# Optimization experiments

Measured on AMD Instinct MI355X. Metric: run time of the kernel, lower is better.

Reference implementation:

```python
import jax, jax.numpy as jnp
import numpy as np

COMMITMENT_COST = 0.25
NUM_EMBEDDINGS = 1024
EMBEDDING_DIM = 256


def setup_inputs() -> dict:
    key = jax.random.key(0)
    k1, k2 = jax.random.split(key)
    inputs = jax.random.normal(k1, (64, 256, 32, 32), dtype=jnp.float32)
    emb_w = jax.random.normal(k2, (NUM_EMBEDDINGS, EMBEDDING_DIM), dtype=jnp.float32)
    return {"inputs": inputs, "emb_w": emb_w}


def reference(inputs, emb_w):
    # NCHW -> NHWC, flatten to [N, D]
    x = jnp.transpose(inputs, (0, 2, 3, 1))  # [B, H, W, D]
    B, H, W, D = x.shape
    flat = x.reshape(-1, D)  # [N, D]

    distances = (
        jnp.sum(flat * flat, axis=1, keepdims=True)
        + jnp.sum(emb_w * emb_w, axis=1)
        - 2.0 * flat @ emb_w.T
    )
    idx = jnp.argmin(distances, axis=1)  # [N]

    # one-hot @ W is just a gather of codebook rows
    quantized = emb_w[idx].reshape(B, H, W, D)

    # avg_probs = mean of one-hot encodings = normalized codeword counts
    counts = jnp.zeros((NUM_EMBEDDINGS,), dtype=jnp.float32).at[idx].add(1.0)
    avg_probs = counts / flat.shape[0]
    perplexity = jnp.exp(-jnp.sum(avg_probs * jnp.log(avg_probs + 1e-10)))

    e_latent_loss = jnp.mean((jax.lax.stop_gradient(quantized) - x) ** 2)
    loss = COMMITMENT_COST * e_latent_loss

    # straight-through estimator
    quantized_st = x + jax.lax.stop_gradient(quantized - x)
    quantized_out = jnp.transpose(quantized_st, (0, 3, 1, 2))  # back to NCHW

    return loss, quantized_out, perplexity, idx.reshape(B, H, W)
```

## Files before the change

### kernel.cpp

```cpp
#include <hip/hip_runtime.h>
#include <hip/hip_bf16.h>
#include <math.h>

typedef _Float16 f16;
typedef __attribute__((ext_vector_type(8))) _Float16 f16x8;
typedef __attribute__((ext_vector_type(16))) float f32x16;

#define DIMS 256
#define NCODE 1024
#define NPTS 65536

#define OUT_Q_OFF 1
#define OUT_PERP_OFF 16777217
#define OUT_IDX_OFF 16777218

#define EHI_F32_OFF 4
#define ELO_F32_OFF (4 + 131072)
#define TILE_BYTES 16384

#define XSTRIDE 132

__device__ __forceinline__ void gload_lds16(const void* g, void* l) {
    __builtin_amdgcn_global_load_lds(
        (const __attribute__((address_space(1))) unsigned int*)g,
        (__attribute__((address_space(3))) unsigned int*)l, 16, 0, 0);
}

__global__ __launch_bounds__(256) void k_eprep(const float* __restrict__ ew,
                                               char* __restrict__ ehi,
                                               char* __restrict__ elo,
                                               float* __restrict__ enorm) {
    int w = threadIdx.x >> 6;
    int l = threadIdx.x & 63;
    int row = blockIdx.x * 4 + w;
    float4 v = *reinterpret_cast<const float4*>(ew + (size_t)row * DIMS + l * 4);
    float vv[4] = {v.x, v.y, v.z, v.w};
    __align__(8) f16 hh[4];
    __align__(8) f16 ll[4];
    float s = 0.0f;
    #pragma unroll
    for (int e = 0; e < 4; ++e) {
        f16 h = (f16)vv[e];
        hh[e] = h;
        ll[e] = (f16)(vv[e] - (float)h);
        s += vv[e] * vv[e];
    }
    size_t off = (size_t)(row >> 5) * TILE_BYTES + (size_t)(row & 31) * 512
               + (size_t)((((l >> 1) ^ (row & 7)) << 4) + ((l & 1) << 3));
    *reinterpret_cast<float2*>(ehi + off) = *reinterpret_cast<float2*>(hh);
    *reinterpret_cast<float2*>(elo + off) = *reinterpret_cast<float2*>(ll);
    #pragma unroll
    for (int off2 = 32; off2 > 0; off2 >>= 1) s += __shfl_down(s, off2);
    if (l == 0) enorm[row] = s;
}

__global__ __launch_bounds__(256, 2) void k_argmin_mfma(const float* __restrict__ x,
                                                        const char* __restrict__ ehi,
                                                        const char* __restrict__ elo,
                                                        const float* __restrict__ enorm,
                                                        int* __restrict__ out_idx) {
    __shared__ __align__(16) char smem[2 * 2 * TILE_BYTES];
    __shared__ float enorm_lds[NCODE];
    float* Xs = (float*)smem;

    const int t = threadIdx.x;
    const int wave = t >> 6;
    const int lane = t & 63;
    const int lrow = lane & 31;
    const int lhalf = lane >> 5;

    const int blk = blockIdx.x;
    const int b = blk >> 3;
    const int hw0 = (blk & 7) << 7;
    const float* xb = x + (size_t)b * (DIMS * 1024) + hw0;

    #pragma unroll
    for (int i = 0; i < 4; ++i) enorm_lds[t + 256 * i] = enorm[t + 256 * i];

    f16x8 ahi[16], alo[16];
    #pragma unroll
    for (int dc = 0; dc < 4; ++dc) {
        __syncthreads();
        #pragma unroll
        for (int i = 0; i < 8; ++i) {
            int d = (t >> 5) + 8 * i;
            int p4 = (t & 31) * 4;
            float4 v = *reinterpret_cast<const float4*>(xb + (size_t)(dc * 64 + d) * 1024 + p4);
            *reinterpret_cast<float4*>(&Xs[d * XSTRIDE + p4]) = v;
        }
        __syncthreads();
        int p = wave * 32 + lrow;
        #pragma unroll
        for (int kcl = 0; kcl < 4; ++kcl) {
            f16x8 h, l;
            #pragma unroll
            for (int e = 0; e < 8; ++e) {
                float xv = Xs[(kcl * 16 + lhalf * 8 + e) * XSTRIDE + p];
                f16 hi = (f16)xv;
                h[e] = hi;
                l[e] = (f16)(xv - (float)hi);
            }
            ahi[dc * 4 + kcl] = h;
            alo[dc * 4 + kcl] = l;
        }
    }
    __syncthreads();

    const char* gplane = (wave >> 1) ? elo : ehi;
    const int pl_off = (wave >> 1) * TILE_BYTES;
    const int woff = (wave & 1) * 8192;

    #pragma unroll
    for (int i = 0; i < 8; ++i) {
        int off = woff + i * 1024;
        gload_lds16(gplane + off + lane * 16, smem + pl_off + off);
    }
    __syncthreads();

    float bestv[16];
    int besti[16];
    #pragma unroll
    for (int r = 0; r < 16; ++r) { bestv[r] = -3.4e38f; besti[r] = 0; }

#define ROUND_BODY(ACC_CUR, ACC_PREV, RD)                                         \
    {                                                                             \
        const int rd_ = (RD);                                                     \
        const int cur_ = rd_ & 1;                                                 \
        if (rd_ + 1 < 32) {                                                       \
            const char* gp_ = gplane + (size_t)(rd_ + 1) * TILE_BYTES;            \
            char* lp_ = smem + (cur_ ^ 1) * (2 * TILE_BYTES) + pl_off;            \
            _Pragma("unroll")                                                     \
            for (int i_ = 0; i_ < 8; ++i_) {                                      \
                int off_ = woff + i_ * 1024;                                      \
                gload_lds16(gp_ + off_ + lane * 16, lp_ + off_);                  \
            }                                                                     \
        }                                                                         \
        const char* EHb_ = smem + cur_ * (2 * TILE_BYTES);                        \
        const char* ELb_ = EHb_ + TILE_BYTES;                                     \
        float nh_ = -0.5f * enorm_lds[rd_ * 32 + lrow];                           \
        _Pragma("unroll")                                                         \
        for (int r_ = 0; r_ < 16; ++r_) ACC_CUR[r_] = nh_;                        \
        __builtin_amdgcn_s_setprio(1);                                            \
        _Pragma("unroll")                                                         \
        for (int kc_ = 0; kc_ < 16; ++kc_) {                                      \
            int g_ = kc_ * 2 + lhalf;                                             \
            int ra_ = lrow * 512 + ((g_ ^ (lrow & 7)) << 4);                      \
            f16x8 bh_ = *reinterpret_cast<const f16x8*>(EHb_ + ra_);              \
            f16x8 bl_ = *reinterpret_cast<const f16x8*>(ELb_ + ra_);              \
            ACC_CUR = __builtin_amdgcn_mfma_f32_32x32x16_f16(ahi[kc_], bh_, ACC_CUR, 0, 0, 0); \
            ACC_CUR = __builtin_amdgcn_mfma_f32_32x32x16_f16(ahi[kc_], bl_, ACC_CUR, 0, 0, 0); \
            ACC_CUR = __builtin_amdgcn_mfma_f32_32x32x16_f16(alo[kc_], bh_, ACC_CUR, 0, 0, 0); \
        }                                                                         \
        __builtin_amdgcn_s_setprio(0);                                            \
        if (rd_ > 0) {                                                            \
            const int cw_ = (rd_ - 1) * 32 + lrow;                                \
            _Pragma("unroll")                                                     \
            for (int r_ = 0; r_ < 16; ++r_) {                                     \
                float s_ = ACC_PREV[r_];                                          \
                if (s_ > bestv[r_]) { bestv[r_] = s_; besti[r_] = cw_; }          \
            }                                                                     \
        }                                                                         \
        __syncthreads();                                                          \
    }

    f32x16 accA, accB;
    for (int rr = 0; rr < 16; ++rr) {
        ROUND_BODY(accA, accB, 2 * rr);
        ROUND_BODY(accB, accA, 2 * rr + 1);
    }
    {
        int cw = 31 * 32 + lrow;
        #pragma unroll
        for (int r = 0; r < 16; ++r) {
            float s = accB[r];
            if (s > bestv[r]) { bestv[r] = s; besti[r] = cw; }
        }
    }
#undef ROUND_BODY

    #pragma unroll
    for (int off = 1; off <= 16; off <<= 1) {
        #pragma unroll
        for (int r = 0; r < 16; ++r) {
            float ov = __shfl_xor(bestv[r], off);
            int oi = __shfl_xor(besti[r], off);
            if (ov > bestv[r] || (ov == bestv[r] && oi < besti[r])) {
                bestv[r] = ov;
                besti[r] = oi;
            }
        }
    }
    if (lrow == 0) {
        #pragma unroll
        for (int r = 0; r < 16; ++r) {
            int row = (r & 3) + 8 * (r >> 2) + 4 * lhalf;
            out_idx[blk * 128 + wave * 32 + row] = besti[r];
        }
    }
}

#define QSTRIDE 258
__global__ __launch_bounds__(512) void k_quant(const float* __restrict__ x,
                                               const float* __restrict__ ew,
                                               const int* __restrict__ idxv,
                                               float* __restrict__ out,
                                               float* __restrict__ loss_acc,
                                               int* __restrict__ counts) {
    __shared__ float Eq[64 * QSTRIDE];
    __shared__ int ids[64];
    __shared__ int h[NCODE];
    const int t = threadIdx.x;
    const int blk = blockIdx.x;
    const int b = blk >> 4;
    const int hw0 = (blk & 15) << 6;

    if (t < 64) ids[t] = idxv[(b << 10) + hw0 + t];
    h[t] = 0;
    if (t < 512) h[t + 512] = 0;
    __syncthreads();

    if (t < 64) atomicAdd(&h[ids[t]], 1);

    #pragma unroll
    for (int i = 0; i < 8; ++i) {
        int f = i * 512 + t;
        int row = f >> 6;
        int c4 = f & 63;
        float4 v = *reinterpret_cast<const float4*>(ew + (size_t)ids[row] * DIMS + c4 * 4);
        float2 lo2 = {v.x, v.y};
        float2 hi2 = {v.z, v.w};
        *reinterpret_cast<float2*>(&Eq[row * QSTRIDE + c4 * 4]) = lo2;
        *reinterpret_cast<float2*>(&Eq[row * QSTRIDE + c4 * 4 + 2]) = hi2;
    }
    __syncthreads();

    const int q4 = t & 15;
    const int cb = t >> 4;
    const int p = q4 * 4;
    float lsum = 0.0f;
    #pragma unroll
    for (int k = 0; k < 8; ++k) {
        int c = k * 32 + cb;
        unsigned g = ((unsigned)b << 18) | ((unsigned)c << 10) | (unsigned)(hw0 + p);
        float4 xv = *reinterpret_cast<const float4*>(x + g);
        float q0 = Eq[(p + 0) * QSTRIDE + c];
        float q1 = Eq[(p + 1) * QSTRIDE + c];
        float q2 = Eq[(p + 2) * QSTRIDE + c];
        float q3 = Eq[(p + 3) * QSTRIDE + c];
        float d0 = q0 - xv.x, d1 = q1 - xv.y, d2 = q2 - xv.z, d3 = q3 - xv.w;
        out[OUT_Q_OFF + g + 0] = xv.x + d0;
        out[OUT_Q_OFF + g + 1] = xv.y + d1;
        out[OUT_Q_OFF + g + 2] = xv.z + d2;
        out[OUT_Q_OFF + g + 3] = xv.w + d3;
        lsum += d0 * d0 + d1 * d1 + d2 * d2 + d3 * d3;
    }
    #pragma unroll
    for (int off = 32; off > 0; off >>= 1) lsum += __shfl_down(lsum, off);
    if ((t & 63) == 0) atomicAdd(&loss_acc[blk & 63], lsum);

    int v0 = h[t];
    if (v0) atomicAdd(&counts[t], v0);
    if (t < 512) {
        int v1 = h[t + 512];
        if (v1) atomicAdd(&counts[t + 512], v1);
    }
    if (t < 64) out[OUT_IDX_OFF + (b << 10) + hw0 + t] = (float)ids[t];
}

__global__ __launch_bounds__(256) void k_final(const int* __restrict__ counts,
                                               const float* __restrict__ loss_acc,
                                               float* __restrict__ out) {
    int t = threadIdx.x;
    float s = 0.0f;
    #pragma unroll
    for (int i = 0; i < 4; ++i) {
        int cnt = counts[t + 256 * i];
        float p = (float)cnt * (1.0f / 65536.0f);
        s += p * logf(p + 1e-10f);
    }
    #pragma unroll
    for (int off = 32; off > 0; off >>= 1) s += __shfl_down(s, off);
    __shared__ float wsum[4];
    if ((t & 63) == 0) wsum[t >> 6] = s;
    __syncthreads();
    if (t == 0) {
        float S = wsum[0] + wsum[1] + wsum[2] + wsum[3];
        out[OUT_PERP_OFF] = expf(-S);
        float ls = 0.0f;
        for (int i = 0; i < 64; ++i) ls += loss_acc[i];
        out[0] = 0.25f * (ls * (1.0f / 16777216.0f));
    }
}

extern "C" void kernel_launch(void* const* d_in, const int* in_sizes, int n_in,
                              void* d_out, int out_size, void* d_ws, size_t ws_size,
                              hipStream_t stream) {
    const float* x = (const float*)d_in[0];
    const float* ew = (const float*)d_in[1];
    float* out = (float*)d_out;
    float* ws = (float*)d_ws;

    float* loss_acc = ws;
    int* counts = (int*)(ws + 64);
    float* enorm = ws + 64 + 1024;
    int* idxv = (int*)(ws + 64 + 2048);

    char* ehi = (char*)(out + EHI_F32_OFF);
    char* elo = (char*)(out + ELO_F32_OFF);

    hipMemsetAsync(d_ws, 0, (64 + 1024) * sizeof(float), stream);

    k_eprep<<<256, 256, 0, stream>>>(ew, ehi, elo, enorm);
    k_argmin_mfma<<<512, 256, 0, stream>>>(x, ehi, elo, enorm, idxv);
    k_quant<<<1024, 512, 0, stream>>>(x, ew, idxv, out, loss_acc, counts);
    k_final<<<1, 256, 0, stream>>>(counts, loss_acc, out);
}
```

Measured before the change: 172.1 us.

## Double argmin block to 512 threads sharing each codebook tile across 8 waves

The argmin kernel now processes 256 points per block with 8 waves instead of 128 points with 4 waves, halving the grid to 256 blocks. Each codebook tile loaded into LDS is reused by twice as many waves, so each wave issues half as many global-to-LDS loads per round and the total codebook traffic from global/L2 is halved. The X staging is split into two half-passes so the LDS buffer size stays unchanged. The cost is more waves waiting at each barrier and a grid of only 256 blocks, which may leave compute units underused.

```diff
diff --git a/kernel.cpp b/kernel.cpp
--- a/kernel.cpp
+++ b/kernel.cpp
@@ -54,7 +54,7 @@
     if (l == 0) enorm[row] = s;
 }
 
-__global__ __launch_bounds__(256, 2) void k_argmin_mfma(const float* __restrict__ x,
+__global__ __launch_bounds__(512, 2) void k_argmin_mfma(const float* __restrict__ x,
                                                         const char* __restrict__ ehi,
                                                         const char* __restrict__ elo,
                                                         const float* __restrict__ enorm,
@@ -70,48 +70,56 @@
     const int lhalf = lane >> 5;
 
     const int blk = blockIdx.x;
-    const int b = blk >> 3;
-    const int hw0 = (blk & 7) << 7;
+    const int b = blk >> 2;
+    const int hw0 = (blk & 3) << 8;
     const float* xb = x + (size_t)b * (DIMS * 1024) + hw0;
 
-    #pragma unroll
-    for (int i = 0; i < 4; ++i) enorm_lds[t + 256 * i] = enorm[t + 256 * i];
+    enorm_lds[t] = enorm[t];
+    enorm_lds[t + 512] = enorm[t + 512];
 
     f16x8 ahi[16], alo[16];
     #pragma unroll
     for (int dc = 0; dc < 4; ++dc) {
-        __syncthreads();
         #pragma unroll
-        for (int i = 0; i < 8; ++i) {
-            int d = (t >> 5) + 8 * i;
-            int p4 = (t & 31) * 4;
-            float4 v = *reinterpret_cast<const float4*>(xb + (size_t)(dc * 64 + d) * 1024 + p4);
-            *reinterpret_cast<float4*>(&Xs[d * XSTRIDE + p4]) = v;
+        for (int h = 0; h < 2; ++h) {
+            __syncthreads();
+            #pragma unroll
+            for (int i = 0; i < 4; ++i) {
+                int id = i * 512 + t;
+                int d = id >> 5;
+                int p4 = id & 31;
+                float4 v = *reinterpret_cast<const float4*>(
+                    xb + (size_t)(dc * 64 + d) * 1024 + h * 128 + p4 * 4);
+                *reinterpret_cast<float4*>(&Xs[d * XSTRIDE + p4 * 4]) = v;
+            }
+            __syncthreads();
+            if ((wave >> 2) == h) {
+                int p = (wave & 3) * 32 + lrow;
+                #pragma unroll
+                for (int kcl = 0; kcl < 4; ++kcl) {
+                    f16x8 hh, ll;
+                    #pragma unroll
+                    for (int e = 0; e < 8; ++e) {
+                        float xv = Xs[(kcl * 16 + lhalf * 8 + e) * XSTRIDE + p];
+                        f16 hi = (f16)xv;
+                        hh[e] = hi;
+                        ll[e] = (f16)(xv - (float)hi);
+                    }
+                    ahi[dc * 4 + kcl] = hh;
+                    alo[dc * 4 + kcl] = ll;
+                }
+            }
         }
-        __syncthreads();
-        int p = wave * 32 + lrow;
-        #pragma unroll
-        for (int kcl = 0; kcl < 4; ++kcl) {
-            f16x8 h, l;
-            #pragma unroll
-            for (int e = 0; e < 8; ++e) {
-                float xv = Xs[(kcl * 16 + lhalf * 8 + e) * XSTRIDE + p];
-                f16 hi = (f16)xv;
-                h[e] = hi;
-                l[e] = (f16)(xv - (float)hi);
-            }
-            ahi[dc * 4 + kcl] = h;
-            alo[dc * 4 + kcl] = l;
-        }
-    }
-    __syncthreads();
-
-    const char* gplane = (wave >> 1) ? elo : ehi;
-    const int pl_off = (wave >> 1) * TILE_BYTES;
-    const int woff = (wave & 1) * 8192;
-
-    #pragma unroll
-    for (int i = 0; i < 8; ++i) {
+    }
+    __syncthreads();
+
+    const int plane = wave >> 2;
+    const char* gplane = plane ? elo : ehi;
+    const int pl_off = plane * TILE_BYTES;
+    const int woff = (wave & 3) * 4096;
+
+    #pragma unroll
+    for (int i = 0; i < 4; ++i) {
         int off = woff + i * 1024;
         gload_lds16(gplane + off + lane * 16, smem + pl_off + off);
     }
@@ -130,7 +138,7 @@
             const char* gp_ = gplane + (size_t)(rd_ + 1) * TILE_BYTES;            \
             char* lp_ = smem + (cur_ ^ 1) * (2 * TILE_BYTES) + pl_off;            \
             _Pragma("unroll")                                                     \
-            for (int i_ = 0; i_ < 8; ++i_) {                                      \
+            for (int i_ = 0; i_ < 4; ++i_) {                                      \
                 int off_ = woff + i_ * 1024;                                      \
                 gload_lds16(gp_ + off_ + lane * 16, lp_ + off_);                  \
             }                                                                     \
@@ -194,7 +202,7 @@
         #pragma unroll
         for (int r = 0; r < 16; ++r) {
             int row = (r & 3) + 8 * (r >> 2) + 4 * lhalf;
-            out_idx[blk * 128 + wave * 32 + row] = besti[r];
+            out_idx[blk * 256 + wave * 32 + row] = besti[r];
         }
     }
 }
@@ -311,7 +319,7 @@
     hipMemsetAsync(d_ws, 0, (64 + 1024) * sizeof(float), stream);
 
     k_eprep<<<256, 256, 0, stream>>>(ew, ehi, elo, enorm);
-    k_argmin_mfma<<<512, 256, 0, stream>>>(x, ehi, elo, enorm, idxv);
+    k_argmin_mfma<<<256, 512, 0, stream>>>(x, ehi, elo, enorm, idxv);
     k_quant<<<1024, 512, 0, stream>>>(x, ew, idxv, out, loss_acc, counts);
     k_final<<<1, 256, 0, stream>>>(counts, loss_acc, out);
 }
```

After: 166.7 us. 3.1% less time.
